# Kernel tuning notes

Measured on AMD Instinct MI355X. Metric: run time of the kernel, lower is better.

The kernel has to match this reference:

```python
import jax, jax.numpy as jnp
import numpy as np

N_EMBD = 1024
N_HEADS = 16
HEAD_DIM = N_EMBD // N_HEADS


def setup_inputs() -> dict:
    key = jax.random.key(0)
    ks = jax.random.split(key, 5)
    s = 0.02
    return {
        "x": jax.random.normal(ks[0], (4, 2048, N_EMBD), dtype=jnp.float32),
        "w_attn": jax.random.normal(ks[1], (N_EMBD, 3 * N_EMBD), dtype=jnp.float32) * s,
        "b_attn": jnp.zeros((3 * N_EMBD,), dtype=jnp.float32),
        "w_proj": jax.random.normal(ks[2], (N_EMBD, N_EMBD), dtype=jnp.float32) * s,
        "b_proj": jnp.zeros((N_EMBD,), dtype=jnp.float32),
    }


def reference(x, w_attn, b_attn, w_proj, b_proj):
    B, T, C = x.shape
    H, D = N_HEADS, HEAD_DIM
    qkv = x @ w_attn + b_attn                      # [B,T,3C]
    q, k, v = jnp.split(qkv, 3, axis=-1)
    q = q.reshape(B, T, H, D).transpose(0, 2, 1, 3)  # [B,H,T,D]
    k = k.reshape(B, T, H, D).transpose(0, 2, 1, 3)
    v = v.reshape(B, T, H, D).transpose(0, 2, 1, 3)
    # Faithful to source bug: divide by d**(-0.5) == multiply by sqrt(d)
    scale = jnp.asarray(D, x.dtype) ** 0.5
    scores = jnp.einsum("bhqd,bhkd->bhqk", q, k) * scale  # [B,H,T,T]
    causal = jnp.tril(jnp.ones((T, T), dtype=bool))
    scores = jnp.where(causal[None, None], scores, -jnp.inf)
    attn = jax.nn.softmax(scores, axis=-1)
    y = jnp.einsum("bhqk,bhkd->bhqd", attn, v)     # [B,H,T,D]
    y = y.transpose(0, 2, 1, 3).reshape(B, T, C)
    return y @ w_proj + b_proj
```

## Files before the change

### kernel.cpp

```cpp
#include <hip/hip_runtime.h>
#include <cmath>

#define BB 4
#define TT 2048
#define CC 1024
#define HH 16
#define DD 64
#define MM (BB*TT)

typedef _Float16 f16x8 __attribute__((ext_vector_type(8)));
typedef _Float16 f16x4 __attribute__((ext_vector_type(4)));
typedef _Float16 f16x2 __attribute__((ext_vector_type(2)));
typedef float f32x4 __attribute__((ext_vector_type(4)));
typedef unsigned short ushort_t;

#define MFMA16(a,b,c) __builtin_amdgcn_mfma_f32_16x16x16f16(a,b,c,0,0,0)

__device__ __forceinline__ unsigned short f2h(float f) {
    _Float16 h = (_Float16)f;
    return __builtin_bit_cast(unsigned short, h);
}

__device__ __forceinline__ f16x2 cvt_pk(float a, float b) {
    return __builtin_bit_cast(f16x2, __builtin_amdgcn_cvt_pkrtz(a, b));
}

__device__ __forceinline__ void gld16(const void* gsrc, void* ldst) {
    void* g = const_cast<void*>(gsrc);
    __builtin_amdgcn_global_load_lds(
        (__attribute__((address_space(1))) void*)g,
        (__attribute__((address_space(3))) void*)ldst,
        16, 0, 0);
}

__global__ __launch_bounds__(256)
void cvt4_kernel(const float* __restrict__ in, ushort_t* __restrict__ out, long n4) {
    long i = (long)blockIdx.x * blockDim.x + threadIdx.x;
    if (i >= n4) return;
    float4 v = ((const float4*)in)[i];
    ushort4 o;
    o.x = f2h(v.x); o.y = f2h(v.y); o.z = f2h(v.z); o.w = f2h(v.w);
    ((ushort4*)out)[i] = o;
}

__global__ __launch_bounds__(256)
void trcvt_kernel(const float* __restrict__ in, ushort_t* __restrict__ out,
                  int K, int N) {
    __shared__ float T[32][33];
    const int tx = threadIdx.x & 31;
    const int ty = threadIdx.x >> 5;
    const int n0 = blockIdx.x * 32;
    const int k0 = blockIdx.y * 32;
    #pragma unroll
    for (int i = 0; i < 4; ++i)
        T[ty + i * 8][tx] = in[(size_t)(k0 + ty + i * 8) * N + n0 + tx];
    __syncthreads();
    #pragma unroll
    for (int i = 0; i < 4; ++i)
        out[(size_t)(n0 + ty + i * 8) * K + k0 + tx] = f2h(T[tx][ty + i * 8]);
}

template<int N, bool QKV>
__global__ __launch_bounds__(256)
void hgemm_kernel(const ushort_t* __restrict__ A, const ushort_t* __restrict__ Bt,
                  const float* __restrict__ bias, float* __restrict__ out,
                  ushort_t* __restrict__ qh, ushort_t* __restrict__ kh,
                  ushort_t* __restrict__ vh)
{
    const int K = 1024;
    __shared__ ushort_t As[2][128 * 32];
    __shared__ ushort_t Bs[2][128 * 32];

    const int tid  = threadIdx.x;
    const int lane = tid & 63;
    const int wave = tid >> 6;
    const int wm   = (wave & 1) * 64;
    const int wn   = (wave >> 1) * 64;
    const int m0   = blockIdx.y * 128;
    const int n0   = blockIdx.x * 128;
    const int lrow = lane & 15;
    const int quad = lane >> 4;

    unsigned offA[4], offB[4];
    ushort_t* ldsA[4];
    ushort_t* ldsB[4];
    #pragma unroll
    for (int p = 0; p < 4; ++p) {
        const int d   = p * 256 + tid;
        const int blk = d >> 9;
        const int row = (d >> 2) & 127;
        const int c16 = d & 3;
        offA[p] = (unsigned)(m0 + row) * K + blk * 32 + c16 * 8;
        offB[p] = (unsigned)(n0 + row) * K + blk * 32 + c16 * 8;
        ldsA[p] = &As[0][0] + (p * 256 + wave * 64) * 8;
        ldsB[p] = &Bs[0][0] + (p * 256 + wave * 64) * 8;
    }

    f32x4 acc[4][4];
    const f32x4 z = {0.f, 0.f, 0.f, 0.f};
    #pragma unroll
    for (int mt = 0; mt < 4; ++mt)
        #pragma unroll
        for (int nt = 0; nt < 4; ++nt)
            acc[mt][nt] = z;

    for (int kk = 0; kk < K; kk += 64) {
        #pragma unroll
        for (int p = 0; p < 4; ++p) {
            gld16(&A[offA[p] + kk],  ldsA[p]);
            gld16(&Bt[offB[p] + kk], ldsB[p]);
        }
        __syncthreads();

        #pragma unroll
        for (int ks = 0; ks < 2; ++ks) {
            f16x8 af[4], bf[4];
            #pragma unroll
            for (int mt = 0; mt < 4; ++mt)
                af[mt] = *(const f16x8*)&As[ks][(wm + mt * 16 + lrow) * 32 + quad * 8];
            #pragma unroll
            for (int nt = 0; nt < 4; ++nt)
                bf[nt] = *(const f16x8*)&Bs[ks][(wn + nt * 16 + lrow) * 32 + quad * 8];
            #pragma unroll
            for (int mt = 0; mt < 4; ++mt)
                #pragma unroll
                for (int nt = 0; nt < 4; ++nt)
                    acc[mt][nt] = __builtin_amdgcn_mfma_f32_16x16x32_f16(
                        af[mt], bf[nt], acc[mt][nt], 0, 0, 0);
        }
        __syncthreads();
    }

    #pragma unroll
    for (int mt = 0; mt < 4; ++mt) {
        const int rbase = m0 + wm + mt * 16 + quad * 4;
        #pragma unroll
        for (int nt = 0; nt < 4; ++nt) {
            const int col = n0 + wn + nt * 16 + lrow;
            const float bv = bias[col];
            if (QKV) {
                const int which = col >> 10;
                const int c = col & 1023;
                const int h = c >> 6, d = c & 63;
                const int b = rbase >> 11, t0 = rbase & 2047;
                if (which == 2) {
                    ushort4 pk;
                    pk.x = f2h(acc[mt][nt][0] + bv);
                    pk.y = f2h(acc[mt][nt][1] + bv);
                    pk.z = f2h(acc[mt][nt][2] + bv);
                    pk.w = f2h(acc[mt][nt][3] + bv);
                    *(ushort4*)&vh[(((size_t)b * HH + h) * DD + d) * TT + t0] = pk;
                } else {
                    ushort_t* dst = which ? kh : qh;
                    const float sc = which ? 1.0f : 8.0f * 1.44269504088896f;
                    #pragma unroll
                    for (int r = 0; r < 4; ++r)
                        dst[(((size_t)b * HH + h) * TT + t0 + r) * DD + d] =
                            f2h((acc[mt][nt][r] + bv) * sc);
                }
            } else {
                #pragma unroll
                for (int r = 0; r < 4; ++r)
                    out[(size_t)(rbase + r) * N + col] = acc[mt][nt][r] + bv;
            }
        }
    }
}

__global__ __launch_bounds__(512, 4)
void attn_mfma_kernel(const ushort_t* __restrict__ qh, const ushort_t* __restrict__ kh,
                      const ushort_t* __restrict__ vh, ushort_t* __restrict__ yh)
{
    __shared__ ushort_t Ks[2][64 * 72];
    __shared__ ushort_t Vs[2][64 * 72];

    const int pr   = blockIdx.x;
    const int bh   = blockIdx.y;
    const int qtA  = 15 - pr;
    const int qtB  = pr;
    const int itA  = 2 * qtA + 2;
    const int tid  = threadIdx.x;
    const int lane = tid & 63;
    const int w    = tid >> 6;
    const int lrow = lane & 15;
    const int quad = lane >> 4;

    const ushort_t* qbase = qh + (size_t)bh * TT * DD;
    const ushort_t* kbase = kh + (size_t)bh * TT * DD;
    const ushort_t* vbase = vh + (size_t)bh * DD * TT;
    const int b = bh >> 4, h = bh & 15;

    const int ur = tid >> 3;
    const int uc = (tid & 7) * 8;

    int q0w = qtA * 128 + w * 16;
    f16x8 aq0 = *(const f16x8*)&qbase[(size_t)(q0w + lrow) * DD + quad * 8];
    f16x8 aq1 = *(const f16x8*)&qbase[(size_t)(q0w + lrow) * DD + 32 + quad * 8];

    const f32x4 z = {0.f, 0.f, 0.f, 0.f};
    f32x4 o[4] = {z, z, z, z};
    float mi = -1e30f, li = 0.f;

    uint4 kr = *(const uint4*)&kbase[(size_t)ur * DD + uc];
    uint4 vr = *(const uint4*)&vbase[(size_t)ur * TT + uc];

    *(uint4*)&Ks[0][ur * 72 + uc] = kr;
    *(uint4*)&Vs[0][ur * 72 + uc] = vr;
    kr = *(const uint4*)&kbase[(size_t)(64 + ur) * DD + uc];
    vr = *(const uint4*)&vbase[(size_t)ur * TT + 64 + uc];
    __syncthreads();

    for (int i = 0; i < 34; ++i) {
        const int cur = i & 1;
        if (i == itA) {
            #pragma unroll
            for (int r = 0; r < 4; ++r) {
                const float inv = 1.0f / __shfl(li, quad * 4 + r, 64);
                const int t = q0w + quad * 4 + r;
                #pragma unroll
                for (int dt = 0; dt < 4; ++dt)
                    yh[((size_t)b * TT + t) * CC + h * 64 + dt * 16 + lrow] =
                        f2h(o[dt][r] * inv);
            }
            q0w = qtB * 128 + w * 16;
            aq0 = *(const f16x8*)&qbase[(size_t)(q0w + lrow) * DD + quad * 8];
            aq1 = *(const f16x8*)&qbase[(size_t)(q0w + lrow) * DD + 32 + quad * 8];
            #pragma unroll
            for (int dt = 0; dt < 4; ++dt) o[dt] = z;
            mi = -1e30f; li = 0.f;
        }
        const int kt = (i < itA) ? i : i - itA;
        const int kt2 = kt * 64;
        if (kt2 <= q0w + 15) {
            f32x4 sv[4];
            __builtin_amdgcn_s_setprio(1);
            #pragma unroll
            for (int c = 0; c < 4; ++c) {
                f16x8 ka = *(const f16x8*)&Ks[cur][(c * 16 + lrow) * 72 + quad * 8];
                f16x8 kb = *(const f16x8*)&Ks[cur][(c * 16 + lrow) * 72 + 32 + quad * 8];
                sv[c] = __builtin_amdgcn_mfma_f32_16x16x32_f16(ka, aq0, z, 0, 0, 0);
                sv[c] = __builtin_amdgcn_mfma_f32_16x16x32_f16(kb, aq1, sv[c], 0, 0, 0);
            }
            __builtin_amdgcn_s_setprio(0);

            const int qg = q0w + lrow;
            if (kt2 + 63 > q0w) {
                #pragma unroll
                for (int c = 0; c < 4; ++c)
                    #pragma unroll
                    for (int r = 0; r < 4; ++r)
                        if (kt2 + c * 16 + quad * 4 + r > qg) sv[c][r] = -3e38f;
            }
            float mc[4];
            #pragma unroll
            for (int c = 0; c < 4; ++c)
                mc[c] = fmaxf(fmaxf(sv[c][0], sv[c][1]), fmaxf(sv[c][2], sv[c][3]));
            float m = fmaxf(fmaxf(mc[0], mc[1]), fmaxf(mc[2], mc[3]));
            m = fmaxf(m, __shfl_xor(m, 16, 64));
            m = fmaxf(m, __shfl_xor(m, 32, 64));

            if (__any(m > mi + 8.0f)) {
                const float mnew  = fmaxf(mi, m);
                const float alpha = exp2f(mi - mnew);
                mi = mnew;
                li *= alpha;
                #pragma unroll
                for (int r = 0; r < 4; ++r) {
                    const float ar = __shfl(alpha, quad * 4 + r, 64);
                    #pragma unroll
                    for (int dt = 0; dt < 4; ++dt) o[dt][r] *= ar;
                }
            }

            f16x4 ap[4];
            float rc[4];
            #pragma unroll
            for (int c = 0; c < 4; ++c) {
                const float p0 = exp2f(sv[c][0] - mi);
                const float p1 = exp2f(sv[c][1] - mi);
                const float p2 = exp2f(sv[c][2] - mi);
                const float p3 = exp2f(sv[c][3] - mi);
                rc[c] = (p0 + p1) + (p2 + p3);
                const f16x2 lo = cvt_pk(p0, p1);
                const f16x2 hi = cvt_pk(p2, p3);
                ap[c][0] = lo[0]; ap[c][1] = lo[1]; ap[c][2] = hi[0]; ap[c][3] = hi[1];
            }
            float rs = (rc[0] + rc[1]) + (rc[2] + rc[3]);
            rs += __shfl_xor(rs, 16, 64);
            rs += __shfl_xor(rs, 32, 64);
            li += rs;

            __builtin_amdgcn_s_setprio(1);
            #pragma unroll
            for (int dt = 0; dt < 4; ++dt)
                #pragma unroll
                for (int c = 0; c < 4; ++c) {
                    f16x4 vb = *(const f16x4*)&Vs[cur][(dt * 16 + lrow) * 72 + c * 16 + quad * 4];
                    o[dt] = MFMA16(ap[c], vb, o[dt]);
                }
            __builtin_amdgcn_s_setprio(0);
        }

        if (i < 33) {
            const int nxt = cur ^ 1;
            *(uint4*)&Ks[nxt][ur * 72 + uc] = kr;
            *(uint4*)&Vs[nxt][ur * 72 + uc] = vr;
            if (i < 32) {
                const int ni  = i + 2;
                const int nkt = (ni < itA) ? ni : ni - itA;
                const int nb  = nkt * 64;
                kr = *(const uint4*)&kbase[(size_t)(nb + ur) * DD + uc];
                vr = *(const uint4*)&vbase[(size_t)ur * TT + nb + uc];
            }
        }
        __syncthreads();
    }

    #pragma unroll
    for (int r = 0; r < 4; ++r) {
        const float inv = 1.0f / __shfl(li, quad * 4 + r, 64);
        const int t = q0w + quad * 4 + r;
        #pragma unroll
        for (int dt = 0; dt < 4; ++dt)
            yh[((size_t)b * TT + t) * CC + h * 64 + dt * 16 + lrow] =
                f2h(o[dt][r] * inv);
    }
}

extern "C" void kernel_launch(void* const* d_in, const int* in_sizes, int n_in,
                              void* d_out, int out_size, void* d_ws, size_t ws_size,
                              hipStream_t stream) {
    const float* x      = (const float*)d_in[0];
    const float* w_attn = (const float*)d_in[1];
    const float* b_attn = (const float*)d_in[2];
    const float* w_proj = (const float*)d_in[3];
    const float* b_proj = (const float*)d_in[4];
    float* out = (float*)d_out;

    const size_t per = (size_t)BB * HH * TT * DD;
    ushort_t* qh  = (ushort_t*)d_ws;
    ushort_t* kh  = qh + per;
    ushort_t* vh  = kh + per;
    ushort_t* xh  = vh + per;
    ushort_t* yh  = xh;
    ushort_t* wat = xh + (size_t)MM * CC;
    ushort_t* wpt = wat + (size_t)3 * CC * CC;

    cvt4_kernel<<<(MM * CC / 4 + 255) / 256, 256, 0, stream>>>(x, xh, MM * CC / 4);
    trcvt_kernel<<<dim3(3 * CC / 32, CC / 32), 256, 0, stream>>>(w_attn, wat, CC, 3 * CC);
    trcvt_kernel<<<dim3(CC / 32, CC / 32), 256, 0, stream>>>(w_proj, wpt, CC, CC);

    hgemm_kernel<3 * CC, true><<<dim3(3 * CC / 128, MM / 128), 256, 0, stream>>>(
        xh, wat, b_attn, nullptr, qh, kh, vh);

    attn_mfma_kernel<<<dim3(8, BB * HH), 512, 0, stream>>>(qh, kh, vh, yh);

    hgemm_kernel<CC, false><<<dim3(CC / 128, MM / 128), 256, 0, stream>>>(
        yh, wpt, b_proj, out, nullptr, nullptr, nullptr);
}
```

Before: 280.5 us.

## Stage QKV GEMM epilogue through LDS for coalesced stores; merge weight transposes

The QKV GEMM epilogue now writes each wave's 64x64 fp16 tile into a reused LDS scratch region and then copies it out to q/k/v with 16-byte vectorized, contiguous global stores. This replaces the scattered 2-byte stores used for Q and K. The two weight transpose-convert kernels are merged into one launch to save a launch. LDS is unified into one buffer so the scratch can alias the operand tiles after the main loop. This relies on the final syncthreads before reuse and on wave-local ordering via lgkmcnt.

After: 270.4 us. 1.04x faster.

```diff
diff --git a/kernel.cpp b/kernel.cpp
--- a/kernel.cpp
+++ b/kernel.cpp
@@ -44,12 +44,17 @@
 }
 
 __global__ __launch_bounds__(256)
-void trcvt_kernel(const float* __restrict__ in, ushort_t* __restrict__ out,
-                  int K, int N) {
+void trcvt2_kernel(const float* __restrict__ wa, const float* __restrict__ wp,
+                   ushort_t* __restrict__ oa, ushort_t* __restrict__ op) {
     __shared__ float T[32][33];
+    const int K = 1024;
+    const float* in;
+    ushort_t* out;
+    int N, n0;
+    if (blockIdx.x < 96) { in = wa; out = oa; N = 3072; n0 = blockIdx.x * 32; }
+    else                 { in = wp; out = op; N = 1024; n0 = (blockIdx.x - 96) * 32; }
     const int tx = threadIdx.x & 31;
     const int ty = threadIdx.x >> 5;
-    const int n0 = blockIdx.x * 32;
     const int k0 = blockIdx.y * 32;
     #pragma unroll
     for (int i = 0; i < 4; ++i)
@@ -68,8 +73,7 @@
                   ushort_t* __restrict__ vh)
 {
     const int K = 1024;
-    __shared__ ushort_t As[2][128 * 32];
-    __shared__ ushort_t Bs[2][128 * 32];
+    __shared__ ushort_t LDSU[16384];
 
     const int tid  = threadIdx.x;
     const int lane = tid & 63;
@@ -92,8 +96,8 @@
         const int c16 = d & 3;
         offA[p] = (unsigned)(m0 + row) * K + blk * 32 + c16 * 8;
         offB[p] = (unsigned)(n0 + row) * K + blk * 32 + c16 * 8;
-        ldsA[p] = &As[0][0] + (p * 256 + wave * 64) * 8;
-        ldsB[p] = &Bs[0][0] + (p * 256 + wave * 64) * 8;
+        ldsA[p] = &LDSU[0]    + (p * 256 + wave * 64) * 8;
+        ldsB[p] = &LDSU[8192] + (p * 256 + wave * 64) * 8;
     }
 
     f32x4 acc[4][4];
@@ -117,10 +121,10 @@
             f16x8 af[4], bf[4];
             #pragma unroll
             for (int mt = 0; mt < 4; ++mt)
-                af[mt] = *(const f16x8*)&As[ks][(wm + mt * 16 + lrow) * 32 + quad * 8];
+                af[mt] = *(const f16x8*)&LDSU[ks * 4096 + (wm + mt * 16 + lrow) * 32 + quad * 8];
             #pragma unroll
             for (int nt = 0; nt < 4; ++nt)
-                bf[nt] = *(const f16x8*)&Bs[ks][(wn + nt * 16 + lrow) * 32 + quad * 8];
+                bf[nt] = *(const f16x8*)&LDSU[8192 + ks * 4096 + (wn + nt * 16 + lrow) * 32 + quad * 8];
             #pragma unroll
             for (int mt = 0; mt < 4; ++mt)
                 #pragma unroll
@@ -131,34 +135,63 @@
         __syncthreads();
     }
 
-    #pragma unroll
-    for (int mt = 0; mt < 4; ++mt) {
-        const int rbase = m0 + wm + mt * 16 + quad * 4;
-        #pragma unroll
-        for (int nt = 0; nt < 4; ++nt) {
-            const int col = n0 + wn + nt * 16 + lrow;
-            const float bv = bias[col];
-            if (QKV) {
-                const int which = col >> 10;
-                const int c = col & 1023;
-                const int h = c >> 6, d = c & 63;
-                const int b = rbase >> 11, t0 = rbase & 2047;
-                if (which == 2) {
-                    ushort4 pk;
-                    pk.x = f2h(acc[mt][nt][0] + bv);
-                    pk.y = f2h(acc[mt][nt][1] + bv);
-                    pk.z = f2h(acc[mt][nt][2] + bv);
-                    pk.w = f2h(acc[mt][nt][3] + bv);
-                    *(ushort4*)&vh[(((size_t)b * HH + h) * DD + d) * TT + t0] = pk;
-                } else {
-                    ushort_t* dst = which ? kh : qh;
-                    const float sc = which ? 1.0f : 8.0f * 1.44269504088896f;
+    if (QKV) {
+        ushort_t* scr = &LDSU[wave * 4096];
+        const int colw  = n0 + wn;
+        const int which = colw >> 10;
+        const int hh    = (colw & 1023) >> 6;
+        const int rowt  = m0 + wm;
+        const int b2    = rowt >> 11;
+        const int t0w   = rowt & 2047;
+        if (which == 2) {
+            #pragma unroll
+            for (int mt = 0; mt < 4; ++mt)
+                #pragma unroll
+                for (int nt = 0; nt < 4; ++nt) {
+                    const float bv = bias[colw + nt * 16 + lrow];
+                    f16x4 pk;
                     #pragma unroll
                     for (int r = 0; r < 4; ++r)
-                        dst[(((size_t)b * HH + h) * TT + t0 + r) * DD + d] =
+                        pk[r] = (_Float16)(acc[mt][nt][r] + bv);
+                    *(f16x4*)&scr[(nt * 16 + lrow) * 64 + mt * 16 + quad * 4] = pk;
+                }
+            asm volatile("s_waitcnt lgkmcnt(0)" ::: "memory");
+            ushort_t* base = vh + ((size_t)b2 * HH + hh) * DD * TT + t0w;
+            #pragma unroll
+            for (int it = 0; it < 8; ++it) {
+                const int g  = it * 64 + lane;
+                const int dd = g >> 3, cc = (g & 7) * 8;
+                *(uint4*)&base[(size_t)dd * TT + cc] = *(const uint4*)&scr[dd * 64 + cc];
+            }
+        } else {
+            const float sc = which ? 1.0f : 8.0f * 1.44269504088896f;
+            #pragma unroll
+            for (int mt = 0; mt < 4; ++mt)
+                #pragma unroll
+                for (int nt = 0; nt < 4; ++nt) {
+                    const float bv = bias[colw + nt * 16 + lrow];
+                    #pragma unroll
+                    for (int r = 0; r < 4; ++r)
+                        scr[(mt * 16 + quad * 4 + r) * 64 + nt * 16 + lrow] =
                             f2h((acc[mt][nt][r] + bv) * sc);
                 }
-            } else {
+            asm volatile("s_waitcnt lgkmcnt(0)" ::: "memory");
+            ushort_t* dstp = (which ? kh : qh) +
+                             (((size_t)b2 * HH + hh) * TT + t0w) * DD;
+            #pragma unroll
+            for (int it = 0; it < 8; ++it) {
+                const int g = it * 64 + lane;
+                *(uint4*)&dstp[g * 8] = *(const uint4*)&scr[g * 8];
+            }
+        }
+    } else {
+        #pragma unroll
+        for (int mt = 0; mt < 4; ++mt) {
+            const int rbase = m0 + wm + mt * 16 + quad * 4;
+            #pragma unroll
+            for (int nt = 0; nt < 4; ++nt) {
+                const int col = n0 + wn + nt * 16 + lrow;
+                const float bv = bias[col];
                 #pragma unroll
                 for (int r = 0; r < 4; ++r)
                     out[(size_t)(rbase + r) * N + col] = acc[mt][nt][r] + bv;
@@ -347,8 +380,7 @@
     ushort_t* wpt = wat + (size_t)3 * CC * CC;
 
     cvt4_kernel<<<(MM * CC / 4 + 255) / 256, 256, 0, stream>>>(x, xh, MM * CC / 4);
-    trcvt_kernel<<<dim3(3 * CC / 32, CC / 32), 256, 0, stream>>>(w_attn, wat, CC, 3 * CC);
-    trcvt_kernel<<<dim3(CC / 32, CC / 32), 256, 0, stream>>>(w_proj, wpt, CC, CC);
+    trcvt2_kernel<<<dim3(128, 32), 256, 0, stream>>>(w_attn, w_proj, wat, wpt);
 
     hgemm_kernel<3 * CC, true><<<dim3(3 * CC / 128, MM / 128), 256, 0, stream>>>(
         xh, wat, b_attn, nullptr, qh, kh, vh);
```
